# Kernel optimization log

Measured on AMD Instinct MI355X. Metric: run time of the kernel, lower is better.

Reference implementation:

```python
import jax, jax.numpy as jnp
import numpy as np

N_NODES = 50000
N_EDGES = 800000
NUM_IN, NUM_OUT, NUM_HID, NUM_MSG = 1, 1, 30, 200


def _linear_params(key, fan_in, fan_out):
    k1, k2 = jax.random.split(key)
    s = 1.0 / np.sqrt(fan_in)
    W = jax.random.uniform(k1, (fan_in, fan_out), jnp.float32, -s, s)
    b = jax.random.uniform(k2, (fan_out,), jnp.float32, -s, s)
    return W, b


def _layer_params(key, c_in, c_out, c_msg):
    ks = jax.random.split(key, 4)
    W1, b1 = _linear_params(ks[0], c_in, c_out)          # lin_1
    Wm1, bm1 = _linear_params(ks[1], 2 * c_in + 2, c_msg)  # mlp[0]
    Wm2, bm2 = _linear_params(ks[2], c_msg, c_in)          # mlp[2]
    W2, b2 = _linear_params(ks[3], c_in, c_out)          # lin_2
    return W1, b1, Wm1, bm1, Wm2, bm2, W2, b2


def setup_inputs() -> dict:
    key = jax.random.key(0)
    ks = jax.random.split(key, 6)
    features = jax.random.normal(ks[0], (N_NODES, NUM_IN), jnp.float32)
    edges = jax.random.randint(ks[1], (2, N_EDGES), 0, N_NODES, jnp.int64)
    weights = jax.random.normal(ks[2], (N_EDGES, 2), jnp.float32)
    inp = {"features": features, "edges": edges, "weights": weights}
    names = ["W1", "b1", "Wm1", "bm1", "Wm2", "bm2", "W2", "b2"]
    for suf, kk, (ci, co) in zip(["d", "h", "o"], ks[3:6],
                                 [(NUM_IN, NUM_HID), (NUM_HID, NUM_HID), (NUM_HID, NUM_OUT)]):
        ps = _layer_params(kk, ci, co, NUM_MSG)
        for nm, p in zip(names, ps):
            inp[f"{nm}_{suf}"] = p
    return inp


def _mpd(x, src, dst, ea, W1, b1, Wm1, bm1, Wm2, bm2, W2, b2):
    # PyG default flow source_to_target: x_j = x[src], x_i = x[dst], aggregate to dst
    xi = x[dst]
    xj = x[src]
    tmp = jnp.concatenate([xi, xj, ea], axis=1)            # [E, 2*in+2]
    h = jax.nn.relu(tmp @ Wm1 + bm1)                       # [E, msg]
    m = h @ Wm2 + bm2                                      # [E, in]
    msg = (m * (xi - xj)) @ W2 + b2                        # [E, out]
    agg = jax.ops.segment_sum(msg, dst, num_segments=x.shape[0])
    return agg + x @ W1 + b1


def reference(features, edges, weights,
              W1_d, b1_d, Wm1_d, bm1_d, Wm2_d, bm2_d, W2_d, b2_d,
              W1_h, b1_h, Wm1_h, bm1_h, Wm2_h, bm2_h, W2_h, b2_h,
              W1_o, b1_o, Wm1_o, bm1_o, Wm2_o, bm2_o, W2_o, b2_o):
    src, dst = edges[0], edges[1]
    x = jax.nn.relu(_mpd(features, src, dst, weights,
                         W1_d, b1_d, Wm1_d, bm1_d, Wm2_d, bm2_d, W2_d, b2_d))
    for _ in range(3):
        x = jax.nn.relu(_mpd(x, src, dst, weights,
                             W1_h, b1_h, Wm1_h, bm1_h, Wm2_h, bm2_h, W2_h, b2_h))
    return _mpd(x, src, dst, weights,
                W1_o, b1_o, Wm1_o, bm1_o, Wm2_o, bm2_o, W2_o, b2_o)
```

## Files before the change

kernel.cpp:

```cpp
#include <hip/hip_runtime.h>

#define N_NODES 50000
#define N_EDGES 800000
#define C_MSG 200

typedef __bf16 bf16;
typedef __attribute__((ext_vector_type(8))) __bf16 bf16x8;
typedef __attribute__((ext_vector_type(4))) float f32x4;

static __device__ __forceinline__ unsigned int pk_bf16(float a, float b) {
    union { bf16 h[2]; unsigned int u; } cv;
    cv.h[0] = (bf16)a; cv.h[1] = (bf16)b;
    return cv.u;
}

static __device__ __forceinline__ f32x4 MF(bf16x8 a, bf16x8 b, f32x4 c) {
    return __builtin_amdgcn_mfma_f32_16x16x32_bf16(a, b, c, 0, 0, 0);
}

static __device__ void dev_pack_wm1(int tid, const float* W, const float* bm1,
                                    bf16* out) {
    int i = tid & 7, lane = (tid >> 3) & 63, rest = tid >> 9;
    int kt = rest % 2, t = rest / 2;
    int k = kt * 32 + ((lane >> 4) * 8) + i;
    int c = lane & 15;
    int n = (t < 12) ? ((t >> 1) * 32 + 2 * c + (t & 1)) : (192 + c);
    float v = 0.f;
    if (n < C_MSG) {
        if (k < 30)       v = W[k * C_MSG + n];
        else if (k == 30) v = bm1[n];
        else if (k >= 32) v = W[(k - 2) * C_MSG + n];
    }
    out[tid] = (bf16)v;
}

static __device__ void dev_pack_wm2(int tid, const float* W, const float* bm2,
                                    bf16* out) {
    int i = tid & 7, lane = (tid >> 3) & 63, rest = tid >> 9;
    int kt = rest % 7, nt = rest / 7;
    int k = kt * 32 + ((lane >> 4) * 8) + i;
    int n = 2 * (lane & 15) + nt;
    float v = 0.f;
    if (n < 30) {
        if (k < C_MSG)       v = W[k * 30 + n];
        else if (k == C_MSG) v = bm2[n];
    }
    out[tid] = (bf16)v;
}

static __device__ void dev_pack_w2h(int tid, const float* W, const float* b2,
                                    bf16* out) {
    int i = tid & 7, lane = (tid >> 3) & 63, nt = tid >> 9;
    int k = ((lane >> 4) * 8) + i;
    int n = 2 * (lane & 15) + nt;
    float v = 0.f;
    if (n < 30) {
        if (k < 30)       v = W[k * 30 + n];
        else if (k == 30) v = b2[n];
    }
    out[tid] = (bf16)v;
}

static __device__ void dev_pack_w2o(int tid, const float* W, const float* b2,
                                    bf16* out) {
    int i = tid & 7, lane = (tid >> 3) & 63;
    int k = ((lane >> 4) * 8) + i;
    int n = lane & 15;
    float v = 0.f;
    if (n == 0) {
        if (k < 30)       v = W[k];
        else if (k == 30) v = b2[0];
    }
    out[tid] = (bf16)v;
}

static __device__ void dev_pack_sel(int tid, bf16* out) {
    int i = tid & 7, lane = (tid >> 3) & 63, f = tid >> 9;
    int kt = f >> 1, nt = f & 1;
    int kloc = ((lane >> 4) * 8) + i;
    int n = 2 * (lane & 15) + nt;
    float v = (kloc == n && n < 30) ? ((kt & 1) ? -1.f : 1.f) : 0.f;
    out[tid] = (bf16)v;
}

__global__ __launch_bounds__(256) void setup_a(
    const int* __restrict__ dst, int* __restrict__ counts,
    const float* __restrict__ Wm1_h, const float* __restrict__ bm1_h,
    const float* __restrict__ Wm1_o, const float* __restrict__ bm1_o,
    const float* __restrict__ Wm2_h, const float* __restrict__ bm2_h,
    const float* __restrict__ Wm2_o, const float* __restrict__ bm2_o,
    const float* __restrict__ W2_h,  const float* __restrict__ b2_h,
    const float* __restrict__ W2_o,  const float* __restrict__ b2_o,
    const float* __restrict__ Wm1_d,
    bf16* __restrict__ Wm1B_h, bf16* __restrict__ Wm1B_o,
    bf16* __restrict__ Wm2B_h, bf16* __restrict__ Wm2B_o,
    bf16* __restrict__ W2B_h,  bf16* __restrict__ W2B_o,
    bf16* __restrict__ SelB,   float* __restrict__ Wm1T_d,
    const float* __restrict__ features, const float* __restrict__ W1_d,
    const float* __restrict__ b1_d, float* __restrict__ bufA) {
    int b = blockIdx.x, t = threadIdx.x;
    if (b < 3125) {
        int e = b * 256 + t;
        if (e < N_EDGES) atomicAdd(&counts[dst[e]], 1);
    } else if (b < 3311) {
        int pb = b - 3125;
        if (pb < 52)       dev_pack_wm1(pb * 256 + t, Wm1_h, bm1_h, Wm1B_h);
        else if (pb < 104) dev_pack_wm1((pb - 52) * 256 + t, Wm1_o, bm1_o, Wm1B_o);
        else if (pb < 132) dev_pack_wm2((pb - 104) * 256 + t, Wm2_h, bm2_h, Wm2B_h);
        else if (pb < 160) dev_pack_wm2((pb - 132) * 256 + t, Wm2_o, bm2_o, Wm2B_o);
        else if (pb < 164) dev_pack_w2h((pb - 160) * 256 + t, W2_h, b2_h, W2B_h);
        else if (pb < 166) dev_pack_w2o((pb - 164) * 256 + t, W2_o, b2_o, W2B_o);
        else if (pb < 182) dev_pack_sel((pb - 166) * 256 + t, SelB);
        else {
            int i = (pb - 182) * 256 + t;
            if (i < C_MSG * 4) Wm1T_d[i] = Wm1_d[(i & 3) * C_MSG + (i >> 2)];
        }
    } else {
        int n = (b - 3311) * 256 + t;
        if (n < N_NODES) {
            float xv = features[n];
            for (int o = 0; o < 30; ++o)
                bufA[n * 30 + o] = fmaf(xv, W1_d[o], b1_d[o]);
        }
    }
}

__global__ __launch_bounds__(256) void scan_kernel(const int* __restrict__ counts,
                                                   int* __restrict__ offsets,
                                                   int* __restrict__ cursor) {
    __shared__ int ws[4];
    const int b = blockIdx.x, t = threadIdx.x;
    const int lane = t & 63, wv = t >> 6;
    int acc = 0;
    for (int i = t; i < b * 256; i += 256) acc += counts[i];
#pragma unroll
    for (int d = 32; d > 0; d >>= 1) acc += __shfl_xor(acc, d);
    if (lane == 0) ws[wv] = acc;
    __syncthreads();
    int base = ws[0] + ws[1] + ws[2] + ws[3];
    __syncthreads();
    int i = b * 256 + t;
    int v = (i < N_NODES) ? counts[i] : 0;
    int inc = v;
#pragma unroll
    for (int d = 1; d < 64; d <<= 1) {
        int u = __shfl_up(inc, d);
        if (lane >= d) inc += u;
    }
    if (lane == 63) ws[wv] = inc;
    __syncthreads();
    int waveoff = 0;
    for (int k = 0; k < wv; ++k) waveoff += ws[k];
    int excl = base + waveoff + inc - v;
    if (i < N_NODES) { offsets[i] = excl; cursor[i] = excl; }
    if (i == N_NODES - 1) offsets[N_NODES] = excl + v;
}

__global__ __launch_bounds__(256) void scatter_kernel(
    const int* __restrict__ src, const int* __restrict__ dst,
    const float* __restrict__ ew, int* __restrict__ cursor,
    int4* __restrict__ edata, float2* __restrict__ ewp) {
    int e = blockIdx.x * 256 + threadIdx.x;
    if (e < N_EDGES) {
        int d = dst[e];
        float e0 = ew[2 * e], e1 = ew[2 * e + 1];
        int p = atomicAdd(&cursor[d], 1);
        edata[p] = make_int4(src[e], d, (int)pk_bf16(e0, e1), e);
        ewp[p] = make_float2(e0, e1);
    }
}

__global__ __launch_bounds__(256) void edge_d_kernel(
    const float* __restrict__ x, const int4* __restrict__ edata,
    const float2* __restrict__ ewp,
    const float* __restrict__ Wm1T, const float* __restrict__ bm1,
    const float* __restrict__ Wm2, const float* __restrict__ bm2,
    const float* __restrict__ W2, const float* __restrict__ b2, bf16* __restrict__ msg)
{
    __shared__ float sw[C_MSG * 6 + 1];
    for (int i = threadIdx.x; i < C_MSG * 6 + 1; i += 256) {
        float v;
        if (i < C_MSG * 4)            v = Wm1T[i];
        else if (i < C_MSG * 5)       v = bm1[i - C_MSG * 4];
        else if (i < C_MSG * 6)       v = Wm2[i - C_MSG * 5];
        else                          v = bm2[0];
        sw[i] = v;
    }
    __syncthreads();

    int t = blockIdx.x * 256 + threadIdx.x;
    int4 ed = edata[t];
    float xi = x[ed.y], xj = x[ed.x];
    float2 e01 = ewp[t];
    float e0 = e01.x, e1 = e01.y;
    float m = sw[C_MSG * 6];
#pragma unroll 4
    for (int j = 0; j < C_MSG; ++j) {
        const float* wr = sw + j * 4;
        float h = sw[C_MSG * 4 + j];
        h = fmaf(xi, wr[0], h);
        h = fmaf(xj, wr[1], h);
        h = fmaf(e0, wr[2], h);
        h = fmaf(e1, wr[3], h);
        h = fmaxf(h, 0.f);
        m = fmaf(h, sw[C_MSG * 5 + j], m);
    }
    float md = m * (xi - xj);
    for (int o = 0; o < 15; ++o) {
        float f0 = fmaf(md, W2[2 * o], b2[2 * o]);
        float f1 = fmaf(md, W2[2 * o + 1], b2[2 * o + 1]);
        *(unsigned int*)(msg + (size_t)t * 32 + 2 * o) = pk_bf16(f0, f1);
    }
}


#define LOAD_FRAGS(P, ED) do {                                                \
    const bf16* rd_ = xc + (size_t)(ED).y * 64 + quad * 8;                    \
    const bf16* rs_ = xc + (size_t)(ED).x * 64 + quad * 8;                    \
    P##A0 = *(const bf16x8*)(rd_);                                            \
    P##a2 = *(const bf16x8*)(rd_ + 32);                                       \
    P##A1 = *(const bf16x8*)(rs_);                                            \
    P##a3 = *(const bf16x8*)(rs_ + 32);                                       \
} while (0)

#define COMPUTE_TILE(P, EDZ, EBASE) do {                                      \
    if (quad == 3) {                                                          \
        union { unsigned int u; bf16 b[2]; } cv_;                             \
        cv_.u = (unsigned int)(EDZ);                                          \
        P##A1[6] = cv_.b[0];                                                  \
        P##A1[7] = cv_.b[1];                                                  \
    }                                                                         \
               \
    f32x4 m0_ = {0.f,0.f,0.f,0.f}, m1_ = {0.f,0.f,0.f,0.f};                   \
    _Pragma("unroll")                                                         \
    for (int p_ = 0; p_ < 6; ++p_) {                                          \
        char* cb_ = (p_ & 1) ? cB : cA;                                       \
        const bf16* Wf_ = Wm1L + (4 * p_) * 512 + lane * 8;                   \
        bf16x8 be0_ = *(const bf16x8*)(Wf_);                                  \
        bf16x8 be1_ = *(const bf16x8*)(Wf_ + 512);                            \
        bf16x8 bo0_ = *(const bf16x8*)(Wf_ + 1024);                           \
        bf16x8 bo1_ = *(const bf16x8*)(Wf_ + 1536);                           \
        f32x4 ae_ = {0.f,0.f,0.f,0.f}, ao_ = {0.f,0.f,0.f,0.f};               \
        ae_ = MF(P##A0, be0_, ae_);                                           \
        ae_ = MF(P##A1, be1_, ae_);                                           \
        ao_ = MF(P##A0, bo0_, ao_);                                           \
        ao_ = MF(P##A1, bo1_, ao_);                                           \
        _Pragma("unroll")                                                     \
        for (int rg_ = 0; rg_ < 4; ++rg_) {                                   \
            int row_ = row0 + rg_, wb_ = 4 * col;                             \
            unsigned int u_ = pk_bf16(fmaxf(ae_[rg_],0.f), fmaxf(ao_[rg_],0.f)); \
            *(unsigned int*)(cb_ + row_ * 64 + ((wb_ & 48) ^ ((row_ & 3) << 4)) \
                             + (wb_ & 15)) = u_;                              \
        }                                                                     \
        bf16x8 a_ = *(const bf16x8*)(cb_ + col * 64 +                         \
                                     ((quad << 4) ^ ((col & 3) << 4)));       \
        m0_ = MF(a_, *(const bf16x8*)(Wm2L + p_ * 512 + lane * 8), m0_);      \
        m1_ = MF(a_, *(const bf16x8*)(Wm2L + (7 + p_) * 512 + lane * 8), m1_);\
    }                                                                         \
    {     \
        const bf16* Wf_ = Wm1L + 24 * 512 + lane * 8;                         \
        bf16x8 b0_ = *(const bf16x8*)(Wf_);                                   \
        bf16x8 b1_ = *(const bf16x8*)(Wf_ + 512);                             \
        f32x4 acc_ = {0.f,0.f,0.f,0.f};                                       \
        acc_ = MF(P##A0, b0_, acc_);                                          \
        acc_ = MF(P##A1, b1_, acc_);                                          \
        if (col < 8) {                                                        \
            _Pragma("unroll")                                                 \
            for (int rg_ = 0; rg_ < 4; ++rg_) {                               \
                int row_ = row0 + rg_;                                        \
                *(bf16*)(cP + row_ * 64 + ((row_ & 3) << 4) + 2 * col) =      \
                    (bf16)fmaxf(acc_[rg_], 0.f);                              \
            }                                                                 \
        }                                                                     \
        bf16x8 a_ = *(const bf16x8*)(cP + col * 64 +                          \
                                     ((quad << 4) ^ ((col & 3) << 4)));       \
        m0_ = MF(a_, *(const bf16x8*)(Wm2L + 6 * 512 + lane * 8), m0_);       \
        m1_ = MF(a_, *(const bf16x8*)(Wm2L + 13 * 512 + lane * 8), m1_);      \
    }                                                                         \
          \
    f32x4 dc0_ = {0.f,0.f,0.f,0.f}, dc1_ = {0.f,0.f,0.f,0.f};                 \
    dc0_ = MF(P##A0, *(const bf16x8*)(SelB + (size_t)0*512 + lane*8), dc0_);  \
    dc1_ = MF(P##A0, *(const bf16x8*)(SelB + (size_t)1*512 + lane*8), dc1_);  \
    dc0_ = MF(P##A1, *(const bf16x8*)(SelB + (size_t)2*512 + lane*8), dc0_);  \
    dc1_ = MF(P##A1, *(const bf16x8*)(SelB + (size_t)3*512 + lane*8), dc1_);  \
    dc0_ = MF(P##a2, *(const bf16x8*)(SelB + (size_t)4*512 + lane*8), dc0_);  \
    dc1_ = MF(P##a2, *(const bf16x8*)(SelB + (size_t)5*512 + lane*8), dc1_);  \
    dc0_ = MF(P##a3, *(const bf16x8*)(SelB + (size_t)6*512 + lane*8), dc0_);  \
    dc1_ = MF(P##a3, *(const bf16x8*)(SelB + (size_t)7*512 + lane*8), dc1_);  \
                                   \
    _Pragma("unroll")                                                         \
    for (int rg_ = 0; rg_ < 4; ++rg_) {                                       \
        int row_ = row0 + rg_, wb_ = 4 * col;                                 \
        unsigned int u_ = (col == 15) ? pk_bf16(1.f, 0.f)                     \
                        : pk_bf16(m0_[rg_]*dc0_[rg_], m1_[rg_]*dc1_[rg_]);    \
        *(unsigned int*)(cA + row_ * 64 + ((wb_ & 48) ^ ((row_ & 3) << 4))    \
                         + (wb_ & 15)) = u_;                                  \
    }                                                                         \
    bf16x8 am_ = *(const bf16x8*)(cA + col * 64 +                             \
                                  ((quad << 4) ^ ((col & 3) << 4)));          \
                                      \
    if (COUT == 30) {                                                         \
        f32x4 c0_ = {0.f,0.f,0.f,0.f}, c1_ = {0.f,0.f,0.f,0.f};               \
        c0_ = MF(am_, *(const bf16x8*)(W2B + lane*8), c0_);                   \
        c1_ = MF(am_, *(const bf16x8*)(W2B + 512 + lane*8), c1_);             \
        _Pragma("unroll")                                                     \
        for (int rg_ = 0; rg_ < 4; ++rg_)                                     \
            *(unsigned int*)(msg + (size_t)((EBASE) + row0 + rg_)*32 + 2*col) = \
                pk_bf16(c0_[rg_], c1_[rg_]);                                  \
    } else {                                                                  \
                  \
        f32x4 c0_ = {0.f,0.f,0.f,0.f};                                        \
        c0_ = MF(am_, *(const bf16x8*)(W2B + lane*8), c0_);                   \
        if (col == 0) {                                                       \
            union { bf16 h[4]; unsigned long long u; } pk4_;                  \
            _Pragma("unroll")                                                 \
            for (int rg_ = 0; rg_ < 4; ++rg_) pk4_.h[rg_] = (bf16)c0_[rg_];   \
            *(unsigned long long*)(msg + ((EBASE) + row0)) = pk4_.u;          \
        }                                                                     \
    }                                                                         \
} while (0)

template<int COUT>
__global__ __launch_bounds__(256, 3) void edge_mfma(
    const bf16* __restrict__ xc, const int4* __restrict__ edata,
    const bf16* __restrict__ Wm1B, const bf16* __restrict__ SelB,
    const bf16* __restrict__ Wm2B, const bf16* __restrict__ W2B,
    bf16* __restrict__ msg)
{
    __shared__ __align__(16) bf16 smem[26624];
    bf16* Wm1L = smem;
    bf16* Wm2L = smem + 13312;

    const int tid = threadIdx.x, w = tid >> 6, lane = tid & 63;
    const int col = lane & 15, quad = lane >> 4, row0 = quad * 4;
    const int myrow = w * 16;
    const int blk = blockIdx.x * 512;

    const int eoff = myrow + col;
    int4 ed0 = edata[blk + 0 * 64 + eoff];
    int4 ed1 = edata[blk + 1 * 64 + eoff];
    int4 ed2 = edata[blk + 2 * 64 + eoff];
    int4 ed3 = edata[blk + 3 * 64 + eoff];
    int4 ed4 = edata[blk + 4 * 64 + eoff];
    int4 ed5 = edata[blk + 5 * 64 + eoff];
    int4 ed6 = edata[blk + 6 * 64 + eoff];
    int4 ed7 = edata[blk + 7 * 64 + eoff];

#pragma unroll
    for (int i = 0; i < 10; ++i) {
        int idx = tid + i * 256;
        bf16x8 v = (idx < 1664) ? *((const bf16x8*)Wm1B + idx)
                                : *((const bf16x8*)Wm2B + (idx - 1664));
        *((bf16x8*)smem + idx) = v;
    }
    __syncthreads();

    char* cbase = (char*)(smem + 20480 + w * 1536);
    char* cA = cbase;
    char* cB = cbase + 1024;
    char* cP = cbase + 2048;

    if (lane < 48) {
        int r = lane / 3, s = 1 + (lane - r * 3);
        bf16x8 z = {};
        if (s == 1) z[0] = (bf16)1.f;
        *(bf16x8*)(cP + r * 64 + ((s << 4) ^ ((r & 3) << 4))) = z;
    }

    bf16x8 pA0, pA1, pa2, pa3, qA0, qA1, qa2, qa3;
    LOAD_FRAGS(p, ed0);
    LOAD_FRAGS(q, ed1);

    COMPUTE_TILE(p, ed0.z, blk + 0 * 64 + myrow);
    LOAD_FRAGS(p, ed2);
    COMPUTE_TILE(q, ed1.z, blk + 1 * 64 + myrow);
    LOAD_FRAGS(q, ed3);
    COMPUTE_TILE(p, ed2.z, blk + 2 * 64 + myrow);
    LOAD_FRAGS(p, ed4);
    COMPUTE_TILE(q, ed3.z, blk + 3 * 64 + myrow);
    LOAD_FRAGS(q, ed5);
    COMPUTE_TILE(p, ed4.z, blk + 4 * 64 + myrow);
    LOAD_FRAGS(p, ed6);
    COMPUTE_TILE(q, ed5.z, blk + 5 * 64 + myrow);
    LOAD_FRAGS(q, ed7);
    COMPUTE_TILE(p, ed6.z, blk + 6 * 64 + myrow);
    COMPUTE_TILE(q, ed7.z, blk + 7 * 64 + myrow);
}

template<int CNEXT>
__global__ __launch_bounds__(256) void agg_fused(
    const bf16* __restrict__ msg, const int* __restrict__ offsets,
    const float* __restrict__ bufc,
    const float* __restrict__ W1n, const float* __restrict__ b1n,
    float* __restrict__ bufn,
    bf16* __restrict__ xc) {
    int gh = (blockIdx.x * 256 + threadIdx.x) >> 4;
    int lane = threadIdx.x & 15;
    int s0 = offsets[gh], s1 = offsets[gh + 1];
    float r0 = 0.f, r1 = 0.f;
    if (lane < 15) {
        float v0 = 0.f, v1 = 0.f;
        const unsigned int* mp =
            (const unsigned int*)(msg + (size_t)s0 * 32 + lane * 2);
        int cnt = s1 - s0, j = 0;
        for (; j + 8 <= cnt; j += 8) {
            unsigned int u0 = mp[(size_t)(j + 0) * 16];
            unsigned int u1 = mp[(size_t)(j + 1) * 16];
            unsigned int u2 = mp[(size_t)(j + 2) * 16];
            unsigned int u3 = mp[(size_t)(j + 3) * 16];
            unsigned int u4 = mp[(size_t)(j + 4) * 16];
            unsigned int u5 = mp[(size_t)(j + 5) * 16];
            unsigned int u6 = mp[(size_t)(j + 6) * 16];
            unsigned int u7 = mp[(size_t)(j + 7) * 16];
            union { unsigned int u; bf16 b[2]; } c0, c1, c2, c3, c4, c5, c6, c7;
            c0.u = u0; c1.u = u1; c2.u = u2; c3.u = u3;
            c4.u = u4; c5.u = u5; c6.u = u6; c7.u = u7;
            v0 += (float)c0.b[0]; v1 += (float)c0.b[1];
            v0 += (float)c1.b[0]; v1 += (float)c1.b[1];
            v0 += (float)c2.b[0]; v1 += (float)c2.b[1];
            v0 += (float)c3.b[0]; v1 += (float)c3.b[1];
            v0 += (float)c4.b[0]; v1 += (float)c4.b[1];
            v0 += (float)c5.b[0]; v1 += (float)c5.b[1];
            v0 += (float)c6.b[0]; v1 += (float)c6.b[1];
            v0 += (float)c7.b[0]; v1 += (float)c7.b[1];
        }
        for (; j + 4 <= cnt; j += 4) {
            unsigned int u0 = mp[(size_t)(j + 0) * 16];
            unsigned int u1 = mp[(size_t)(j + 1) * 16];
            unsigned int u2 = mp[(size_t)(j + 2) * 16];
            unsigned int u3 = mp[(size_t)(j + 3) * 16];
            union { unsigned int u; bf16 b[2]; } c0, c1, c2, c3;
            c0.u = u0; c1.u = u1; c2.u = u2; c3.u = u3;
            v0 += (float)c0.b[0]; v1 += (float)c0.b[1];
            v0 += (float)c1.b[0]; v1 += (float)c1.b[1];
            v0 += (float)c2.b[0]; v1 += (float)c2.b[1];
            v0 += (float)c3.b[0]; v1 += (float)c3.b[1];
        }
        for (; j < cnt; ++j) {
            union { unsigned int u; bf16 b[2]; } cv;
            cv.u = mp[(size_t)j * 16];
            v0 += (float)cv.b[0]; v1 += (float)cv.b[1];
        }
        float f0 = bufc[(size_t)gh * 30 + 2 * lane] + v0;
        float f1 = bufc[(size_t)gh * 30 + 2 * lane + 1] + v1;
        r0 = fmaxf(f0, 0.f);
        r1 = fmaxf(f1, 0.f);
        bf16 h0 = (bf16)r0, h1 = (bf16)r1;
        union { bf16 h[2]; unsigned int u; } hi;
        hi.h[0] = h0; hi.h[1] = h1;
        *(unsigned int*)(xc + (size_t)gh * 64 + 2 * lane) = hi.u;
        *(unsigned int*)(xc + (size_t)gh * 64 + 32 + 2 * lane) =
            pk_bf16(r0 - (float)h0, r1 - (float)h1);
    } else {
        *(unsigned int*)(xc + (size_t)gh * 64 + 30) = pk_bf16(1.f, 0.f);
        *(unsigned int*)(xc + (size_t)gh * 64 + 62) = 0u;
    }
    if (CNEXT == 30) {
        float acc0 = 0.f, acc1 = 0.f;
        if (lane < 15) { acc0 = b1n[2 * lane]; acc1 = b1n[2 * lane + 1]; }
        for (int k2 = 0; k2 < 15; ++k2) {
            float rk0 = __shfl(r0, k2, 16);
            float rk1 = __shfl(r1, k2, 16);
            if (lane < 15) {
                const float* w0 = W1n + (2 * k2) * 30 + 2 * lane;
                const float* w1 = W1n + (2 * k2 + 1) * 30 + 2 * lane;
                acc0 = fmaf(rk0, w0[0], acc0);
                acc1 = fmaf(rk0, w0[1], acc1);
                acc0 = fmaf(rk1, w1[0], acc0);
                acc1 = fmaf(rk1, w1[1], acc1);
            }
        }
        if (lane < 15) {
            bufn[(size_t)gh * 30 + 2 * lane] = acc0;
            bufn[(size_t)gh * 30 + 2 * lane + 1] = acc1;
        }
    } else {
        float acc = b1n[0];
        for (int k2 = 0; k2 < 15; ++k2) {
            float rk0 = __shfl(r0, k2, 16);
            float rk1 = __shfl(r1, k2, 16);
            acc = fmaf(rk0, W1n[2 * k2], acc);
            acc = fmaf(rk1, W1n[2 * k2 + 1], acc);
        }
        if (lane == 0) bufn[gh] = acc;
    }
}

__global__ __launch_bounds__(256) void agg_last(const bf16* __restrict__ msg1,
                                                const int* __restrict__ offsets,
                                                float* __restrict__ out) {
    int gh = (blockIdx.x * 256 + threadIdx.x) >> 5;
    int lane = threadIdx.x & 31;
    int s0 = offsets[gh], s1 = offsets[gh + 1];
    float v = 0.f;
    for (int j = s0 + lane; j < s1; j += 32) v += (float)msg1[j];
#pragma unroll
    for (int o = 16; o > 0; o >>= 1) v += __shfl_xor(v, o);
    if (lane == 0) out[gh] += v;
}

extern "C" void kernel_launch(void* const* d_in, const int* in_sizes, int n_in,
                              void* d_out, int out_size, void* d_ws, size_t ws_size,
                              hipStream_t stream) {
    const float* features = (const float*)d_in[0];
    const int*   edges    = (const int*)d_in[1];
    const float* ew       = (const float*)d_in[2];

    const float* W1_d  = (const float*)d_in[3];
    const float* b1_d  = (const float*)d_in[4];
    const float* Wm1_d = (const float*)d_in[5];
    const float* bm1_d = (const float*)d_in[6];
    const float* Wm2_d = (const float*)d_in[7];
    const float* bm2_d = (const float*)d_in[8];
    const float* W2_d  = (const float*)d_in[9];
    const float* b2_d  = (const float*)d_in[10];

    const float* W1_h  = (const float*)d_in[11];
    const float* b1_h  = (const float*)d_in[12];
    const float* Wm1_h = (const float*)d_in[13];
    const float* bm1_h = (const float*)d_in[14];
    const float* Wm2_h = (const float*)d_in[15];
    const float* bm2_h = (const float*)d_in[16];
    const float* W2_h  = (const float*)d_in[17];
    const float* b2_h  = (const float*)d_in[18];

    const float* W1_o  = (const float*)d_in[19];
    const float* b1_o  = (const float*)d_in[20];
    const float* Wm1_o = (const float*)d_in[21];
    const float* bm1_o = (const float*)d_in[22];
    const float* Wm2_o = (const float*)d_in[23];
    const float* bm2_o = (const float*)d_in[24];
    const float* W2_o  = (const float*)d_in[25];
    const float* b2_o  = (const float*)d_in[26];

    const int* src = edges;
    const int* dst = edges + N_EDGES;
    float* out = (float*)d_out;

    char* p = (char*)d_ws;
    auto alloc = [&](size_t bytes) { char* r = p; p += (bytes + 63) & ~(size_t)63; return r; };
    float* bufA    = (float*)alloc((size_t)N_NODES * 30 * 4);
    float* bufB    = (float*)alloc((size_t)N_NODES * 30 * 4);
    bf16*  msg     = (bf16*) alloc((size_t)(N_EDGES + 256) * 32 * 2);
    bf16*  xc      = (bf16*) alloc((size_t)N_NODES * 64 * 2);
    int*   counts  = (int*)  alloc((size_t)N_NODES * 4);
    int*   offsets = (int*)  alloc((size_t)(N_NODES + 1) * 4);
    int*   cursor  = (int*)  alloc((size_t)N_NODES * 4);
    int4*  edata   = (int4*) alloc((size_t)(N_EDGES + 256) * 16);
    float2* ewp    = (float2*)alloc((size_t)N_EDGES * 8);
    float* Wm1T_d  = (float*)alloc((size_t)C_MSG * 4 * 4);
    bf16*  Wm1B_h  = (bf16*) alloc((size_t)26 * 512 * 2);
    bf16*  Wm1B_o  = (bf16*) alloc((size_t)26 * 512 * 2);
    bf16*  Wm2B_h  = (bf16*) alloc((size_t)14 * 512 * 2);
    bf16*  Wm2B_o  = (bf16*) alloc((size_t)14 * 512 * 2);
    bf16*  W2B_h   = (bf16*) alloc((size_t)2 * 512 * 2);
    bf16*  W2B_o   = (bf16*) alloc((size_t)1 * 512 * 2);
    bf16*  SelB    = (bf16*) alloc((size_t)8 * 512 * 2);

    hipMemsetAsync(counts, 0, (size_t)N_NODES * 4, stream);
    hipMemsetAsync(edata + N_EDGES, 0, (size_t)256 * 16, stream);
    setup_a<<<3507, 256, 0, stream>>>(dst, counts,
        Wm1_h, bm1_h, Wm1_o, bm1_o, Wm2_h, bm2_h, Wm2_o, bm2_o,
        W2_h, b2_h, W2_o, b2_o, Wm1_d,
        Wm1B_h, Wm1B_o, Wm2B_h, Wm2B_o, W2B_h, W2B_o, SelB, Wm1T_d,
        features, W1_d, b1_d, bufA);
    scan_kernel<<<(N_NODES + 255) / 256, 256, 0, stream>>>(counts, offsets, cursor);
    scatter_kernel<<<N_EDGES / 256, 256, 0, stream>>>(src, dst, ew, cursor, edata, ewp);

    dim3 tb(256);
    dim3 eb_mfma((N_EDGES + 511) / 512);
    dim3 eb_valu(N_EDGES / 256);
    dim3 ab16(N_NODES * 16 / 256);
    dim3 ab32(N_NODES * 32 / 256);

    edge_d_kernel<<<eb_valu, tb, 0, stream>>>(features, edata, ewp,
        Wm1T_d, bm1_d, Wm2_d, bm2_d, W2_d, b2_d, msg);
    agg_fused<30><<<ab16, tb, 0, stream>>>(msg, offsets, bufA, W1_h, b1_h, bufB, xc);

    edge_mfma<30><<<eb_mfma, tb, 0, stream>>>(xc, edata,
        Wm1B_h, SelB, Wm2B_h, W2B_h, msg);
    agg_fused<30><<<ab16, tb, 0, stream>>>(msg, offsets, bufB, W1_h, b1_h, bufA, xc);

    edge_mfma<30><<<eb_mfma, tb, 0, stream>>>(xc, edata,
        Wm1B_h, SelB, Wm2B_h, W2B_h, msg);
    agg_fused<30><<<ab16, tb, 0, stream>>>(msg, offsets, bufA, W1_h, b1_h, bufB, xc);

    edge_mfma<30><<<eb_mfma, tb, 0, stream>>>(xc, edata,
        Wm1B_h, SelB, Wm2B_h, W2B_h, msg);
    agg_fused<1><<<ab16, tb, 0, stream>>>(msg, offsets, bufB, W1_o, b1_o, out, xc);

    edge_mfma<1><<<eb_mfma, tb, 0, stream>>>(xc, edata,
        Wm1B_o, SelB, Wm2B_o, W2B_o, msg);
    agg_last<<<ab32, tb, 0, stream>>>(msg, offsets, out);
}
```

Measured before the change: 582.8 us.

## Halve edges per MFMA block, remap blocks across XCDs, raise MFMA wave priority

Each edge_mfma block now handles 256 edges instead of 512, which doubles the grid to N_EDGES/256 blocks and removes the padding memset and padded buffers. Block IDs are remapped so that consecutive edge chunks land on the same XCD, which is meant to improve L2 locality for the CSR-sorted edge data and the gathered node features. s_setprio raises wave priority around the MFMA compute section so that matrix work is favoured over other waves' memory phases. In exchange, each block reloads the full weight set into LDS for half as many edges, roughly doubling the fixed per-block staging cost.

```diff
diff --git a/kernel.cpp b/kernel.cpp
--- a/kernel.cpp
+++ b/kernel.cpp
@@ -230,6 +230,7 @@
         P##A1[6] = cv_.b[0];                                                  \
         P##A1[7] = cv_.b[1];                                                  \
     }                                                                         \
+    __builtin_amdgcn_s_setprio(1);                                            \
                \
     f32x4 m0_ = {0.f,0.f,0.f,0.f}, m1_ = {0.f,0.f,0.f,0.f};                   \
     _Pragma("unroll")                                                         \
@@ -303,6 +304,7 @@
         f32x4 c0_ = {0.f,0.f,0.f,0.f}, c1_ = {0.f,0.f,0.f,0.f};               \
         c0_ = MF(am_, *(const bf16x8*)(W2B + lane*8), c0_);                   \
         c1_ = MF(am_, *(const bf16x8*)(W2B + 512 + lane*8), c1_);             \
+        __builtin_amdgcn_s_setprio(0);                                        \
         _Pragma("unroll")                                                     \
         for (int rg_ = 0; rg_ < 4; ++rg_)                                     \
             *(unsigned int*)(msg + (size_t)((EBASE) + row0 + rg_)*32 + 2*col) = \
@@ -311,6 +313,7 @@
                   \
         f32x4 c0_ = {0.f,0.f,0.f,0.f};                                        \
         c0_ = MF(am_, *(const bf16x8*)(W2B + lane*8), c0_);                   \
+        __builtin_amdgcn_s_setprio(0);                                        \
         if (col == 0) {                                                       \
             union { bf16 h[4]; unsigned long long u; } pk4_;                  \
             _Pragma("unroll")                                                 \
@@ -334,24 +337,26 @@
     const int tid = threadIdx.x, w = tid >> 6, lane = tid & 63;
     const int col = lane & 15, quad = lane >> 4, row0 = quad * 4;
     const int myrow = w * 16;
-    const int blk = blockIdx.x * 512;
+
+    const int nblk = gridDim.x;
+    const int q = nblk >> 3, r = nblk & 7;
+    const int xcd = blockIdx.x & 7, idx = blockIdx.x >> 3;
+    const int sbid = (xcd < r) ? (xcd * (q + 1) + idx)
+                               : (r * (q + 1) + (xcd - r) * q + idx);
+    const int blk = sbid * 256;
 
     const int eoff = myrow + col;
     int4 ed0 = edata[blk + 0 * 64 + eoff];
     int4 ed1 = edata[blk + 1 * 64 + eoff];
     int4 ed2 = edata[blk + 2 * 64 + eoff];
     int4 ed3 = edata[blk + 3 * 64 + eoff];
-    int4 ed4 = edata[blk + 4 * 64 + eoff];
-    int4 ed5 = edata[blk + 5 * 64 + eoff];
-    int4 ed6 = edata[blk + 6 * 64 + eoff];
-    int4 ed7 = edata[blk + 7 * 64 + eoff];
 
 #pragma unroll
     for (int i = 0; i < 10; ++i) {
-        int idx = tid + i * 256;
-        bf16x8 v = (idx < 1664) ? *((const bf16x8*)Wm1B + idx)
-                                : *((const bf16x8*)Wm2B + (idx - 1664));
-        *((bf16x8*)smem + idx) = v;
+        int idxs = tid + i * 256;
+        bf16x8 v = (idxs < 1664) ? *((const bf16x8*)Wm1B + idxs)
+                                 : *((const bf16x8*)Wm2B + (idxs - 1664));
+        *((bf16x8*)smem + idxs) = v;
     }
     __syncthreads();
 
@@ -361,10 +366,10 @@
     char* cP = cbase + 2048;
 
     if (lane < 48) {
-        int r = lane / 3, s = 1 + (lane - r * 3);
+        int rr = lane / 3, s = 1 + (lane - rr * 3);
         bf16x8 z = {};
         if (s == 1) z[0] = (bf16)1.f;
-        *(bf16x8*)(cP + r * 64 + ((s << 4) ^ ((r & 3) << 4))) = z;
+        *(bf16x8*)(cP + rr * 64 + ((s << 4) ^ ((rr & 3) << 4))) = z;
     }
 
     bf16x8 pA0, pA1, pa2, pa3, qA0, qA1, qa2, qa3;
@@ -376,15 +381,7 @@
     COMPUTE_TILE(q, ed1.z, blk + 1 * 64 + myrow);
     LOAD_FRAGS(q, ed3);
     COMPUTE_TILE(p, ed2.z, blk + 2 * 64 + myrow);
-    LOAD_FRAGS(p, ed4);
     COMPUTE_TILE(q, ed3.z, blk + 3 * 64 + myrow);
-    LOAD_FRAGS(q, ed5);
-    COMPUTE_TILE(p, ed4.z, blk + 4 * 64 + myrow);
-    LOAD_FRAGS(p, ed6);
-    COMPUTE_TILE(q, ed5.z, blk + 5 * 64 + myrow);
-    LOAD_FRAGS(q, ed7);
-    COMPUTE_TILE(p, ed6.z, blk + 6 * 64 + myrow);
-    COMPUTE_TILE(q, ed7.z, blk + 7 * 64 + myrow);
 }
 
 template<int CNEXT>
@@ -541,12 +538,12 @@
     auto alloc = [&](size_t bytes) { char* r = p; p += (bytes + 63) & ~(size_t)63; return r; };
     float* bufA    = (float*)alloc((size_t)N_NODES * 30 * 4);
     float* bufB    = (float*)alloc((size_t)N_NODES * 30 * 4);
-    bf16*  msg     = (bf16*) alloc((size_t)(N_EDGES + 256) * 32 * 2);
+    bf16*  msg     = (bf16*) alloc((size_t)N_EDGES * 32 * 2);
     bf16*  xc      = (bf16*) alloc((size_t)N_NODES * 64 * 2);
     int*   counts  = (int*)  alloc((size_t)N_NODES * 4);
     int*   offsets = (int*)  alloc((size_t)(N_NODES + 1) * 4);
     int*   cursor  = (int*)  alloc((size_t)N_NODES * 4);
-    int4*  edata   = (int4*) alloc((size_t)(N_EDGES + 256) * 16);
+    int4*  edata   = (int4*) alloc((size_t)N_EDGES * 16);
     float2* ewp    = (float2*)alloc((size_t)N_EDGES * 8);
     float* Wm1T_d  = (float*)alloc((size_t)C_MSG * 4 * 4);
     bf16*  Wm1B_h  = (bf16*) alloc((size_t)26 * 512 * 2);
@@ -558,7 +555,6 @@
     bf16*  SelB    = (bf16*) alloc((size_t)8 * 512 * 2);
 
     hipMemsetAsync(counts, 0, (size_t)N_NODES * 4, stream);
-    hipMemsetAsync(edata + N_EDGES, 0, (size_t)256 * 16, stream);
     setup_a<<<3507, 256, 0, stream>>>(dst, counts,
         Wm1_h, bm1_h, Wm1_o, bm1_o, Wm2_h, bm2_h, Wm2_o, bm2_o,
         W2_h, b2_h, W2_o, b2_o, Wm1_d,
@@ -568,7 +564,7 @@
     scatter_kernel<<<N_EDGES / 256, 256, 0, stream>>>(src, dst, ew, cursor, edata, ewp);
 
     dim3 tb(256);
-    dim3 eb_mfma((N_EDGES + 511) / 512);
+    dim3 eb_mfma(N_EDGES / 256);
     dim3 eb_valu(N_EDGES / 256);
     dim3 ab16(N_NODES * 16 / 256);
     dim3 ab32(N_NODES * 32 / 256);
```

Measured after the change: 581.6 us. About the same (-0.2%).
